# Optimization experiments

Measured on AMD Instinct MI355X. Metric: run time of the kernel, lower is better.

Reference implementation:

```python
import jax, jax.numpy as jnp
import numpy as np

D_MODEL = 1024
NUM_HEADS = 16
D_K = D_MODEL // NUM_HEADS


def setup_inputs() -> dict:
    key = jax.random.key(0)
    ks = jax.random.split(key, 11)
    B, S = 2, 2048
    scale = 1.0 / np.sqrt(D_MODEL)
    inp = {
        "Q": jax.random.normal(ks[0], (B, S, D_MODEL), jnp.float32),
        "K": jax.random.normal(ks[1], (B, S, D_MODEL), jnp.float32),
        "V": jax.random.normal(ks[2], (B, S, D_MODEL), jnp.float32),
        "W_q": jax.random.normal(ks[3], (D_MODEL, D_MODEL), jnp.float32) * scale,
        "b_q": jnp.zeros((D_MODEL,), jnp.float32),
        "W_k": jax.random.normal(ks[4], (D_MODEL, D_MODEL), jnp.float32) * scale,
        "b_k": jnp.zeros((D_MODEL,), jnp.float32),
        "W_v": jax.random.normal(ks[5], (D_MODEL, D_MODEL), jnp.float32) * scale,
        "b_v": jnp.zeros((D_MODEL,), jnp.float32),
        "W_o": jax.random.normal(ks[6], (D_MODEL, D_MODEL), jnp.float32) * scale,
        "b_o": jnp.zeros((D_MODEL,), jnp.float32),
    }
    return inp


def _split_heads(x):
    # [B, S, D] -> [B, H, S, d_k]
    B, S, _ = x.shape
    return x.reshape(B, S, NUM_HEADS, D_K).transpose(0, 2, 1, 3)


def reference(Q, K, V, W_q, b_q, W_k, b_k, W_v, b_v, W_o, b_o):
    # linear projections (torch Linear: x @ W.T + b)
    q = _split_heads(Q @ W_q.T + b_q)
    k = _split_heads(K @ W_k.T + b_k)
    v = _split_heads(V @ W_v.T + b_v)
    # scaled dot-product attention, full [B,H,S,S] scores as in source
    scores = jnp.einsum("bhqd,bhkd->bhqk", q, k) / jnp.sqrt(jnp.float32(D_K))
    probs = jax.nn.softmax(scores, axis=-1)
    ctx = jnp.einsum("bhqk,bhkd->bhqd", probs, v)
    # combine heads: [B,H,S,d_k] -> [B,S,D]
    B, H, S, d = ctx.shape
    ctx = ctx.transpose(0, 2, 1, 3).reshape(B, S, H * d)
    return ctx @ W_o.T + b_o
```

## Files before the change

kernel.cpp:

```cpp
#include <hip/hip_runtime.h>
#include <hip/hip_bf16.h>

typedef unsigned short u16;
typedef unsigned int u32;
typedef short s16x8 __attribute__((ext_vector_type(8)));
typedef float f32x4 __attribute__((ext_vector_type(4)));
typedef float f32x16 __attribute__((ext_vector_type(16)));
typedef u32 u32x4 __attribute__((ext_vector_type(4)));

#define DEV static __device__ __forceinline__

DEV u16 bf16_rne(float f) {
  u32 u = __builtin_bit_cast(u32, f);
  u += 0x7fffu + ((u >> 16) & 1u);
  return (u16)(u >> 16);
}

#define GLDS16(g, l)                                                           \
  __builtin_amdgcn_global_load_lds(                                           \
      (const __attribute__((address_space(1))) void*)(g),                     \
      (__attribute__((address_space(3))) void*)(l), 16, 0, 0)

__global__ void cvt4_kernel(const float* s0, const float* s1, const float* s2,
                            const float* s3, u16* d0, u16* d1, u16* d2,
                            u16* d3, int n4) {
  const int z = blockIdx.y;
  const float* s = (z == 0) ? s0 : (z == 1) ? s1 : (z == 2) ? s2 : s3;
  u16* d = (z == 0) ? d0 : (z == 1) ? d1 : (z == 2) ? d2 : d3;
  int i = blockIdx.x * blockDim.x + threadIdx.x;
  if (i < n4) {
    float4 v = reinterpret_cast<const float4*>(s)[i];
    ushort4 o;
    o.x = bf16_rne(v.x);
    o.y = bf16_rne(v.y);
    o.z = bf16_rne(v.z);
    o.w = bf16_rne(v.w);
    reinterpret_cast<ushort4*>(d)[i] = o;
  }
}

__global__ __launch_bounds__(256, 3) void gemm_qkv(
    const u16* __restrict__ A0, const u16* __restrict__ A1,
    const u16* __restrict__ A2, const u16* __restrict__ W0,
    const u16* __restrict__ W1, const u16* __restrict__ W2,
    const float* __restrict__ bias0, const float* __restrict__ bias1,
    const float* __restrict__ bias2, u16* __restrict__ C0,
    u16* __restrict__ C1v, u16* __restrict__ C2, int M, int N, int K) {
  const int z = blockIdx.z;
  const u16* A = (z == 0) ? A0 : (z == 1) ? A1 : A2;
  const u16* W = (z == 0) ? W0 : (z == 1) ? W1 : W2;
  const float* bias = (z == 0) ? bias0 : (z == 1) ? bias1 : bias2;
  u16* Cout = (z == 0) ? C0 : (z == 1) ? C1v : C2;
  const float escale = (z == 0) ? 0.125f * 1.44269504088896f : 1.0f;

  __shared__ __align__(16) u16 As[128 * 64];
  __shared__ __align__(16) u16 Ws[128 * 64];
  const int tid = threadIdx.x;
  const int lane = tid & 63;
  const int w = tid >> 6;
  const int wr = w >> 1, wc = w & 1;
  const int l15 = lane & 15, l4 = lane >> 4;
  const int m0 = blockIdx.x * 128, n0 = blockIdx.y * 128;

  f32x4 acc[4][4] = {};
  float bv[4];
#pragma unroll
  for (int fc = 0; fc < 4; ++fc) bv[fc] = bias[n0 + wc * 64 + fc * 16 + l15];

  for (int kt = 0; kt < K; kt += 64) {
    __syncthreads();
#pragma unroll
    for (int i = 0; i < 4; ++i) {
      const int ch = i * 256 + tid;
      const int row = ch >> 3, cl = ch & 7;
      GLDS16(A + (size_t)(m0 + row) * K + kt + ((cl ^ (row & 7)) * 8),
             As + (size_t)(i * 256 + w * 64) * 8);
    }
#pragma unroll
    for (int i = 0; i < 4; ++i) {
      const int ch = i * 256 + tid;
      const int row = ch >> 3, cl = ch & 7;
      GLDS16(W + (size_t)(n0 + row) * K + kt + ((cl ^ (row & 7)) * 8),
             Ws + (size_t)(i * 256 + w * 64) * 8);
    }
    __syncthreads();
#pragma unroll
    for (int ks = 0; ks < 2; ++ks) {
      const int sw = (ks * 4 + l4) ^ (l15 & 7);
      s16x8 a[4], b[4];
#pragma unroll
      for (int f = 0; f < 4; ++f)
        a[f] = *(const s16x8*)(As + (size_t)((wr * 64 + f * 16 + l15) * 8 + sw) * 8);
#pragma unroll
      for (int f = 0; f < 4; ++f)
        b[f] = *(const s16x8*)(Ws + (size_t)((wc * 64 + f * 16 + l15) * 8 + sw) * 8);
#pragma unroll
      for (int fr = 0; fr < 4; ++fr)
#pragma unroll
        for (int fc = 0; fc < 4; ++fc)
          acc[fr][fc] = __builtin_amdgcn_mfma_f32_16x16x32_bf16(
              a[fr], b[fc], acc[fr][fc], 0, 0, 0);
    }
  }

  if (z == 2) {
#pragma unroll
    for (int fr = 0; fr < 4; ++fr) {
      const int m = m0 + wr * 64 + fr * 16 + l4 * 4;
      const int bb = m >> 11, s = m & 2047;
#pragma unroll
      for (int fc = 0; fc < 4; ++fc) {
        const int n = n0 + wc * 64 + fc * 16 + l15;
        const int hh = n >> 6, dd = n & 63;
        ushort4 o;
        o.x = bf16_rne(acc[fr][fc][0] + bv[fc]);
        o.y = bf16_rne(acc[fr][fc][1] + bv[fc]);
        o.z = bf16_rne(acc[fr][fc][2] + bv[fc]);
        o.w = bf16_rne(acc[fr][fc][3] + bv[fc]);
        *(ushort4*)(Cout + (((size_t)(bb * 16 + hh) * 64 + dd) * 2048 + s)) = o;
      }
    }
  } else {
#pragma unroll
    for (int fr = 0; fr < 4; ++fr) {
      const int mrow = m0 + wr * 64 + fr * 16 + l4 * 4;
#pragma unroll
      for (int fc = 0; fc < 4; ++fc) {
        const int ncol = n0 + wc * 64 + fc * 16 + l15;
#pragma unroll
        for (int r = 0; r < 4; ++r)
          Cout[(size_t)(mrow + r) * N + ncol] =
              bf16_rne((acc[fr][fc][r] + bv[fc]) * escale);
      }
    }
  }
}

__global__ __launch_bounds__(256, 4) void gemm_o(
    const u16* __restrict__ A, const u16* __restrict__ W,
    const float* __restrict__ bias, float* __restrict__ Cout, int M, int N,
    int K) {
  __shared__ __align__(16) u16 As[128 * 64];
  __shared__ __align__(16) u16 Ws[64 * 64];
  const int tid = threadIdx.x;
  const int lane = tid & 63;
  const int w = tid >> 6;
  const int wr = w >> 1, wc = w & 1;
  const int l15 = lane & 15, l4 = lane >> 4;
  const int m0 = blockIdx.x * 128, n0 = blockIdx.y * 64;

  f32x4 acc[4][2] = {};
  float bv[2];
#pragma unroll
  for (int fc = 0; fc < 2; ++fc) bv[fc] = bias[n0 + wc * 32 + fc * 16 + l15];

  for (int kt = 0; kt < K; kt += 64) {
    __syncthreads();
#pragma unroll
    for (int i = 0; i < 4; ++i) {
      const int ch = i * 256 + tid;
      const int row = ch >> 3, cl = ch & 7;
      GLDS16(A + (size_t)(m0 + row) * K + kt + ((cl ^ (row & 7)) * 8),
             As + (size_t)(i * 256 + w * 64) * 8);
    }
#pragma unroll
    for (int i = 0; i < 2; ++i) {
      const int ch = i * 256 + tid;
      const int row = ch >> 3, cl = ch & 7;
      GLDS16(W + (size_t)(n0 + row) * K + kt + ((cl ^ (row & 7)) * 8),
             Ws + (size_t)(i * 256 + w * 64) * 8);
    }
    __syncthreads();
#pragma unroll
    for (int ks = 0; ks < 2; ++ks) {
      const int sw = (ks * 4 + l4) ^ (l15 & 7);
      s16x8 a[4], b[2];
#pragma unroll
      for (int f = 0; f < 4; ++f)
        a[f] = *(const s16x8*)(As + (size_t)((wr * 64 + f * 16 + l15) * 8 + sw) * 8);
#pragma unroll
      for (int f = 0; f < 2; ++f)
        b[f] = *(const s16x8*)(Ws + (size_t)((wc * 32 + f * 16 + l15) * 8 + sw) * 8);
#pragma unroll
      for (int fr = 0; fr < 4; ++fr)
#pragma unroll
        for (int fc = 0; fc < 2; ++fc)
          acc[fr][fc] = __builtin_amdgcn_mfma_f32_16x16x32_bf16(
              a[fr], b[fc], acc[fr][fc], 0, 0, 0);
    }
  }

#pragma unroll
  for (int fr = 0; fr < 4; ++fr) {
    const int mrow = m0 + wr * 64 + fr * 16 + l4 * 4;
#pragma unroll
    for (int fc = 0; fc < 2; ++fc) {
      const int ncol = n0 + wc * 32 + fc * 16 + l15;
#pragma unroll
      for (int r = 0; r < 4; ++r)
        Cout[(size_t)(mrow + r) * N + ncol] = acc[fr][fc][r] + bv[fc];
    }
  }
}

__global__ __launch_bounds__(512, 4) void attn_fused(
    const u16* __restrict__ qp, const u16* __restrict__ kp,
    const u16* __restrict__ vt, u16* __restrict__ ctx) {
  const int S = 2048, D = 1024;
  const int bh = blockIdx.x;
  const int qt = blockIdx.y;
  const int tid = threadIdx.x, lane = tid & 63, w = tid >> 6;
  const int l31 = lane & 31, l5 = lane >> 5;
  const int g = tid >> 8;
  const int tl = tid & 255;
  const int wl = tl >> 6;
  const int wq = w & 3;

  __shared__ __align__(16) u16 SM[32768];

  const size_t qkbase = ((size_t)(bh >> 4) * S) * D + (size_t)(bh & 15) * 64;
  const size_t vbase = (size_t)bh * 64 * S;

  const int q = qt * 128 + wq * 32 + l31;
  s16x8 qf[4];
#pragma unroll
  for (int ks = 0; ks < 4; ++ks)
    qf[ks] = *(const s16x8*)(qp + qkbase + (size_t)q * D + ks * 16 + l5 * 8);

  u32x4 onesw;
  onesw[0] = onesw[1] = onesw[2] = onesw[3] = 0x3F803F80u;
  const s16x8 ones = __builtin_bit_cast(s16x8, onesw);

  f32x16 octx[2] = {};
  f32x16 lacc = {};

  auto stage = [&](int buf, int ti) {
    const int kv0 = (g * 16 + ti) * 64;
    u16* Kd = SM + g * 16384 + buf * 4096;
    u16* Vd = SM + g * 16384 + 8192 + buf * 4096;
#pragma unroll
    for (int i = 0; i < 2; ++i) {
      const int gch = i * 256 + tl;
      const int kv = gch >> 3, cc = gch & 7;
      GLDS16(kp + qkbase + (size_t)(kv0 + kv) * D + ((cc ^ (kv & 7)) << 3),
             Kd + (size_t)(i * 256 + wl * 64) * 8);
    }
#pragma unroll
    for (int i = 0; i < 2; ++i) {
      const int gch = i * 256 + tl;
      const int d = gch >> 3, cc = gch & 7;
      GLDS16(vt + vbase + (size_t)d * S + kv0 + ((cc ^ (d & 7)) << 3),
             Vd + (size_t)(i * 256 + wl * 64) * 8);
    }
  };

  stage(0, 0);
  const int NT = 16;
  for (int t = 0; t < NT; ++t) {
    __syncthreads();
    if (t + 1 < NT) stage((t + 1) & 1, t + 1);
    const u16* Kb = SM + g * 16384 + (t & 1) * 4096;
    const u16* Vb = SM + g * 16384 + 8192 + (t & 1) * 4096;

    f32x16 sc[2] = {};
#pragma unroll
    for (int ks = 0; ks < 4; ++ks) {
      __builtin_amdgcn_s_setprio(1);
#pragma unroll
      for (int fk = 0; fk < 2; ++fk) {
        const int kv = fk * 32 + l31;
        const int c = (ks << 1) + l5;
        const s16x8 kf =
            *(const s16x8*)(Kb + (size_t)(kv * 8 + (c ^ (kv & 7))) * 8);
        sc[fk] = __builtin_amdgcn_mfma_f32_32x32x16_bf16(kf, qf[ks], sc[fk],
                                                         0, 0, 0);
      }
      __builtin_amdgcn_s_setprio(0);
    }

#pragma unroll
    for (int c4 = 0; c4 < 4; ++c4) {
      const int fk = c4 >> 1, hf = c4 & 1;
      float p[8];
#pragma unroll
      for (int j = 0; j < 8; ++j)
        p[j] = __builtin_amdgcn_exp2f(sc[fk][hf * 8 + j]);
      u32 x0, x1, y0, y1;
      asm("v_cvt_pk_bf16_f32 %0, %1, %2" : "=v"(x0) : "v"(p[0]), "v"(p[1]));
      asm("v_cvt_pk_bf16_f32 %0, %1, %2" : "=v"(x1) : "v"(p[2]), "v"(p[3]));
      asm("v_cvt_pk_bf16_f32 %0, %1, %2" : "=v"(y0) : "v"(p[4]), "v"(p[5]));
      asm("v_cvt_pk_bf16_f32 %0, %1, %2" : "=v"(y1) : "v"(p[6]), "v"(p[7]));
      asm("v_permlane32_swap_b32 %0, %1" : "+v"(x0), "+v"(y0));
      asm("v_permlane32_swap_b32 %0, %1" : "+v"(x1), "+v"(y1));
      u32x4 bw;
      bw[0] = x0; bw[1] = x1; bw[2] = y0; bw[3] = y1;
      const s16x8 pb = __builtin_bit_cast(s16x8, bw);
      __builtin_amdgcn_s_setprio(1);
      lacc = __builtin_amdgcn_mfma_f32_32x32x16_bf16(ones, pb, lacc, 0, 0, 0);
#pragma unroll
      for (int fd = 0; fd < 2; ++fd) {
        const int d = fd * 32 + l31;
        const int c = (c4 << 1) + l5;
        const s16x8 vf =
            *(const s16x8*)(Vb + (size_t)(d * 8 + (c ^ (d & 7))) * 8);
        octx[fd] = __builtin_amdgcn_mfma_f32_32x32x16_bf16(vf, pb, octx[fd],
                                                           0, 0, 0);
      }
      __builtin_amdgcn_s_setprio(0);
    }
  }

  const float lpart = lacc[0];

  __syncthreads();
  float* scr = (float*)(void*)SM;
  if (g == 1) {
    float* dst = scr + ((size_t)wq * 64 + lane) * 33;
#pragma unroll
    for (int fd = 0; fd < 2; ++fd)
#pragma unroll
      for (int r = 0; r < 16; ++r) dst[fd * 16 + r] = octx[fd][r];
    dst[32] = lpart;
  }
  __syncthreads();
  if (g == 0) {
    const float* src = scr + ((size_t)wq * 64 + lane) * 33;
    const float linv = 1.f / (lpart + src[32]);
#pragma unroll
    for (int fd = 0; fd < 2; ++fd)
#pragma unroll
      for (int gg = 0; gg < 4; ++gg) {
        ushort4 o;
        o.x = bf16_rne((octx[fd][gg * 4 + 0] + src[fd * 16 + gg * 4 + 0]) * linv);
        o.y = bf16_rne((octx[fd][gg * 4 + 1] + src[fd * 16 + gg * 4 + 1]) * linv);
        o.z = bf16_rne((octx[fd][gg * 4 + 2] + src[fd * 16 + gg * 4 + 2]) * linv);
        o.w = bf16_rne((octx[fd][gg * 4 + 3] + src[fd * 16 + gg * 4 + 3]) * linv);
        *(ushort4*)(ctx + qkbase + (size_t)q * D + fd * 32 + gg * 8 + l5 * 4) =
            o;
      }
  }
}

extern "C" void kernel_launch(void* const* d_in, const int* in_sizes, int n_in,
                              void* d_out, int out_size, void* d_ws,
                              size_t ws_size, hipStream_t stream) {
  (void)in_sizes; (void)n_in; (void)out_size; (void)ws_size;
  const float* Q = (const float*)d_in[0];
  const float* K = (const float*)d_in[1];
  const float* V = (const float*)d_in[2];
  const float* Wq = (const float*)d_in[3];
  const float* bq = (const float*)d_in[4];
  const float* Wk = (const float*)d_in[5];
  const float* bk = (const float*)d_in[6];
  const float* Wv = (const float*)d_in[7];
  const float* bv = (const float*)d_in[8];
  const float* Wo = (const float*)d_in[9];
  const float* bo = (const float*)d_in[10];

  const int B = 2, S = 2048, D = 1024, H = 16;
  const int M = B * S;
  const size_t NE = (size_t)M * D;
  const size_t WE = (size_t)D * D;

  u16* Qb = (u16*)d_ws;
  u16* Kb = Qb + NE;
  u16* Vb = Kb + NE;
  u16* qp = Vb + NE;
  u16* kp = qp + NE;
  u16* vtb = kp + NE;
  u16* Wqb = vtb + NE;
  u16* Wkb = Wqb + WE;
  u16* Wvb = Wkb + WE;
  u16* Wob = Wvb + WE;

  const int n4 = (int)(NE / 4), nb = (n4 + 255) / 256;
  const int w4 = (int)(WE / 4), wb = (w4 + 255) / 256;
  cvt4_kernel<<<dim3(nb, 3), 256, 0, stream>>>(Q, K, V, nullptr, Qb, Kb, Vb,
                                               nullptr, n4);
  cvt4_kernel<<<dim3(wb, 4), 256, 0, stream>>>(Wq, Wk, Wv, Wo, Wqb, Wkb, Wvb,
                                               Wob, w4);

  dim3 gg(M / 128, D / 128, 3);
  gemm_qkv<<<gg, 256, 0, stream>>>(Qb, Kb, Vb, Wqb, Wkb, Wvb, bq, bk, bv, qp,
                                   kp, vtb, M, D, D);

  dim3 ga(B * H, S / 128);
  attn_fused<<<ga, 512, 0, stream>>>(qp, kp, vtb, Qb);

  dim3 go(M / 128, D / 64);
  gemm_o<<<go, 256, 0, stream>>>(Qb, Wob, bo, (float*)d_out, M, D, D);
}
```

Baseline: 107.5 us.

## Load K/V fragments directly from global memory instead of LDS staging

Removes the double-buffered global-to-LDS staging of K and V tiles and the per-iteration block barriers from the attention kernel. Each wave now reads its K and V MFMA fragments straight from global memory and relies on the L1/L2 caches for reuse across the four waves that share a KV range. LDS is cut to a small float scratch used only for the final cross-group reduction, and the occupancy hint is dropped from the launch bounds. This trades barrier and LDS traffic for redundant, higher-latency global loads that are no longer prefetched a tile ahead.

```diff
diff --git a/kernel.cpp b/kernel.cpp
--- a/kernel.cpp
+++ b/kernel.cpp
@@ -203,7 +203,7 @@
   }
 }
 
-__global__ __launch_bounds__(512, 4) void attn_fused(
+__global__ __launch_bounds__(512) void attn_fused(
     const u16* __restrict__ qp, const u16* __restrict__ kp,
     const u16* __restrict__ vt, u16* __restrict__ ctx) {
   const int S = 2048, D = 1024;
@@ -211,12 +211,10 @@
   const int qt = blockIdx.y;
   const int tid = threadIdx.x, lane = tid & 63, w = tid >> 6;
   const int l31 = lane & 31, l5 = lane >> 5;
-  const int g = tid >> 8;
-  const int tl = tid & 255;
-  const int wl = tl >> 6;
+  const int g = w >> 2;
   const int wq = w & 3;
 
-  __shared__ __align__(16) u16 SM[32768];
+  __shared__ __align__(16) float scr[4 * 64 * 33];
 
   const size_t qkbase = ((size_t)(bh >> 4) * S) * D + (size_t)(bh & 15) * 64;
   const size_t vbase = (size_t)bh * 64 * S;
@@ -234,33 +232,12 @@
   f32x16 octx[2] = {};
   f32x16 lacc = {};
 
-  auto stage = [&](int buf, int ti) {
-    const int kv0 = (g * 16 + ti) * 64;
-    u16* Kd = SM + g * 16384 + buf * 4096;
-    u16* Vd = SM + g * 16384 + 8192 + buf * 4096;
-#pragma unroll
-    for (int i = 0; i < 2; ++i) {
-      const int gch = i * 256 + tl;
-      const int kv = gch >> 3, cc = gch & 7;
-      GLDS16(kp + qkbase + (size_t)(kv0 + kv) * D + ((cc ^ (kv & 7)) << 3),
-             Kd + (size_t)(i * 256 + wl * 64) * 8);
-    }
-#pragma unroll
-    for (int i = 0; i < 2; ++i) {
-      const int gch = i * 256 + tl;
-      const int d = gch >> 3, cc = gch & 7;
-      GLDS16(vt + vbase + (size_t)d * S + kv0 + ((cc ^ (d & 7)) << 3),
-             Vd + (size_t)(i * 256 + wl * 64) * 8);
-    }
-  };
-
-  stage(0, 0);
+  const u16* kbase = kp + qkbase;
+  const u16* vb = vt + vbase;
+
   const int NT = 16;
   for (int t = 0; t < NT; ++t) {
-    __syncthreads();
-    if (t + 1 < NT) stage((t + 1) & 1, t + 1);
-    const u16* Kb = SM + g * 16384 + (t & 1) * 4096;
-    const u16* Vb = SM + g * 16384 + 8192 + (t & 1) * 4096;
+    const int kv0 = g * 1024 + t * 64;
 
     f32x16 sc[2] = {};
 #pragma unroll
@@ -268,10 +245,9 @@
       __builtin_amdgcn_s_setprio(1);
 #pragma unroll
       for (int fk = 0; fk < 2; ++fk) {
-        const int kv = fk * 32 + l31;
-        const int c = (ks << 1) + l5;
+        const int kv = kv0 + fk * 32 + l31;
         const s16x8 kf =
-            *(const s16x8*)(Kb + (size_t)(kv * 8 + (c ^ (kv & 7))) * 8);
+            *(const s16x8*)(kbase + (size_t)kv * D + ks * 16 + l5 * 8);
         sc[fk] = __builtin_amdgcn_mfma_f32_32x32x16_bf16(kf, qf[ks], sc[fk],
                                                          0, 0, 0);
       }
@@ -300,9 +276,8 @@
 #pragma unroll
       for (int fd = 0; fd < 2; ++fd) {
         const int d = fd * 32 + l31;
-        const int c = (c4 << 1) + l5;
-        const s16x8 vf =
-            *(const s16x8*)(Vb + (size_t)(d * 8 + (c ^ (d & 7))) * 8);
+        const s16x8 vf = *(const s16x8*)(vb + (size_t)d * S + kv0 + c4 * 16 +
+                                         l5 * 8);
         octx[fd] = __builtin_amdgcn_mfma_f32_32x32x16_bf16(vf, pb, octx[fd],
                                                            0, 0, 0);
       }
@@ -312,8 +287,6 @@
 
   const float lpart = lacc[0];
 
-  __syncthreads();
-  float* scr = (float*)(void*)SM;
   if (g == 1) {
     float* dst = scr + ((size_t)wq * 64 + lane) * 33;
 #pragma unroll
```

New measurement: 182.8 us. 1.7x slower.
